# Performance work log

Hardware: AMD Instinct MI355X
Metric: run time of the kernel (lower is better)

## Reference

```python
import jax, jax.numpy as jnp
import numpy as np
from jax import lax

GROUPS = 32
CH = 2048
CG = CH // GROUPS  # 64 channels per group
H = W = 64
B = 4
EPS = 1e-5


def _conv2d(x, w, b, padding, dilation=1):
    # x: [N, Cin, H, W], w: [Cout, Cin, kh, kw] (OIHW)
    y = lax.conv_general_dilated(
        x, w, window_strides=(1, 1),
        padding=[(padding, padding), (padding, padding)],
        rhs_dilation=(dilation, dilation),
        dimension_numbers=("NCHW", "OIHW", "NCHW"))
    return y + b[None, :, None, None]


def _prelu(x, alpha):
    # single shared slope (num_parameters=1)
    return jnp.where(x >= 0, x, alpha[0] * x)


def setup_inputs() -> dict:
    key = jax.random.key(0)
    ks = jax.random.split(key, 6)
    s = 0.05
    f32 = jnp.float32
    return {
        "x": jax.random.normal(ks[0], (B, CH, H, W), f32),
        # EFFM.conv1x1 (on concatenated pooled h/w strips)
        "w_hw": jax.random.normal(ks[1], (CG, CG, 1, 1), f32) * s,
        "b_hw": jnp.zeros((CG,), f32),
        # GroupNorm(cg, cg): per-channel affine
        "gn_w": jnp.ones((CG,), f32),
        "gn_b": jnp.zeros((CG,), f32),
        # RC branch1: 3x3 conv pad=1 + PReLU
        "w_b1": jax.random.normal(ks[2], (CG, CG, 3, 3), f32) * s,
        "b_b1": jnp.zeros((CG,), f32),
        "a_b1": jnp.full((1,), 0.25, f32),
        # RC branch2: 3x3 conv dilation=2 pad=2 + PReLU
        "w_b2": jax.random.normal(ks[3], (CG, CG, 3, 3), f32) * s,
        "b_b2": jnp.zeros((CG,), f32),
        "a_b2": jnp.full((1,), 0.25, f32),
        # RC conv128to64: 1x1 conv 2*cg -> cg
        "w_cat": jax.random.normal(ks[4], (CG, 2 * CG, 1, 1), f32) * s,
        "b_cat": jnp.zeros((CG,), f32),
    }


def _effm(x, w_hw, b_hw, gn_w, gn_b, w_b1, b_b1, a_b1, w_b2, b_b2, a_b2, w_cat, b_cat):
    b, c, h, w = x.shape
    cg = c // GROUPS
    bg = b * GROUPS
    gx = x.reshape(bg, cg, h, w)

    # --- coordinate attention branch ---
    x_h = jnp.mean(gx, axis=3, keepdims=True)                       # [bg, cg, h, 1]
    x_w = jnp.mean(gx, axis=2, keepdims=True).transpose(0, 1, 3, 2)  # [bg, cg, w, 1]
    hw = jnp.concatenate([x_h, x_w], axis=2)                         # [bg, cg, h+w, 1]
    # 1x1 conv == channel mixing linear
    hw = jnp.einsum("oi,bilk->bolk", w_hw[:, :, 0, 0], hw) + b_hw[None, :, None, None]
    x_h, x_w = hw[:, :, :h, :], hw[:, :, h:, :]
    gate = gx * jax.nn.sigmoid(x_h) * jax.nn.sigmoid(x_w.transpose(0, 1, 3, 2))

    # GroupNorm(num_groups=cg, num_channels=cg) == per-channel instance norm
    mu = jnp.mean(gate, axis=(2, 3), keepdims=True)
    var = jnp.var(gate, axis=(2, 3), keepdims=True)
    x1 = (gate - mu) * lax.rsqrt(var + EPS)
    x1 = x1 * gn_w[None, :, None, None] + gn_b[None, :, None, None]

    # --- RC multi-scale branch ---
    br1 = _prelu(_conv2d(gx, w_b1, b_b1, padding=1), a_b1) + gx
    br2 = _prelu(_conv2d(gx, w_b2, b_b2, padding=2, dilation=2), a_b2) + gx
    cat = jnp.concatenate([br1, br2], axis=1)                        # [bg, 2cg, h, w]
    x2 = jnp.einsum("oi,bihw->bohw", w_cat[:, :, 0, 0], cat) + b_cat[None, :, None, None]

    # --- cross softmax-matmul attention ---
    x11 = jax.nn.softmax(jnp.mean(x1, axis=(2, 3)), axis=-1)          # [bg, cg]
    x21 = jax.nn.softmax(jnp.mean(x2, axis=(2, 3)), axis=-1)          # [bg, cg]
    weights = (jnp.einsum("gc,gchw->ghw", x11, x2)
               + jnp.einsum("gc,gchw->ghw", x21, x1))                # [bg, h, w]
    out = gx * jax.nn.sigmoid(weights)[:, None, :, :]
    return out.reshape(b, c, h, w)


def reference(x, w_hw, b_hw, gn_w, gn_b, w_b1, b_b1, a_b1, w_b2, b_b2, a_b2, w_cat, b_cat):
    return _effm(x, w_hw, b_hw, gn_w, gn_b, w_b1, b_b1, a_b1, w_b2, b_b2, a_b2, w_cat, b_cat)
```

## Files before the change

kernel.cpp:

```cpp
#include <hip/hip_runtime.h>
#include <hip/hip_bf16.h>

#define HWPX 4096

typedef __attribute__((ext_vector_type(8))) short short8v;
typedef __attribute__((ext_vector_type(4))) float f32x4;
typedef __attribute__((ext_vector_type(16))) float f32x16;
#define MFMA32(a,b,c) __builtin_amdgcn_mfma_f32_32x32x16_bf16(a,b,c,0,0,0)

__device__ __forceinline__ float sigf(float x){ return 1.0f/(1.0f+__expf(-x)); }
__device__ __forceinline__ unsigned short f2bf(float f){
  __hip_bfloat16 h = __float2bfloat16(f);
  unsigned short u; __builtin_memcpy(&u, &h, sizeof(u)); return u;
}
__device__ __forceinline__ float bf2f(unsigned short u){
  return __uint_as_float(((unsigned)u)<<16);
}
__device__ __forceinline__ void gl2lds16(const void* g, void* l){
  __builtin_amdgcn_global_load_lds((const __attribute__((address_space(1))) void*)g,
                                   (__attribute__((address_space(3))) void*)l, 16, 0, 0);
}

__global__ __launch_bounds__(256) void k_pre(const float* __restrict__ x,
                                             const float* __restrict__ wb1,
                                             const float* __restrict__ wb2,
                                             const float* __restrict__ wcat,
                                             const float* __restrict__ gnb,
                                             unsigned short* __restrict__ xb,
                                             float* __restrict__ hwbuf,
                                             unsigned short* __restrict__ wimg,
                                             unsigned short* __restrict__ wcimg,
                                             float* __restrict__ x11,
                                             float* __restrict__ x2mean){
  int bid = blockIdx.x, tid = threadIdx.x;
  if (bid >= 1088){
    int idx = (bid - 1088)*2048 + tid*8;
    f32x4 z = {0.f,0.f,0.f,0.f};
    *(f32x4*)(x2mean + idx) = z;
    *(f32x4*)(x2mean + idx + 4) = z;
    return;
  }
  if (bid >= 1024){
    int bid2 = bid - 1024;
    for (int idx = bid2*256 + tid; idx < 73728; idx += 64*256){
      int f = idx >> 9, r = idx & 511, lane = r >> 3, j = r & 7;
      int ck = f / 36, rem = f % 36;
      int conv = rem / 18, rem2 = rem % 18;
      int tap = rem2 >> 1, cot = rem2 & 1;
      int co = cot*32 + (lane & 31);
      int ci = ck*16 + (lane >> 5)*8 + j;
      const float* src = conv ? wb2 : wb1;
      wimg[idx] = f2bf(src[(co*64 + ci)*9 + tap]);
    }
    if (bid2 == 0){
      for (int idx = tid; idx < 8192; idx += 256){
        int f = idx >> 9, r = idx & 511, lane = r >> 3, j = r & 7;
        int kfc = f >> 1, cot = f & 1;
        int o = cot*32 + (lane & 31);
        int ch = kfc*16 + (lane >> 5)*8 + j;
        wcimg[idx] = f2bf(wcat[o*128 + ch]);
      }
      if (tid < 64){
        float g = gnb[tid];
        float m = g;
        for (int s=32; s; s>>=1) m = fmaxf(m, __shfl_xor(m, s));
        float e = __expf(g-m);
        float se = e;
        for (int s=32; s; s>>=1) se += __shfl_xor(se, s);
        x11[tid] = e/se;
      }
    }
    return;
  }
  int g = bid >> 3, slot = bid & 7;
  int col = tid & 63, wid = tid >> 6;
  __shared__ float rsm[8*64];
  __shared__ float csm[4*8*64];
  float colacc[8] = {0,0,0,0,0,0,0,0};
  const float* xbase = x + ((size_t)(g*64 + slot*8))*HWPX;
  for (int p=0;p<16;++p){
    int r = wid + 4*p;
    const float* src = xbase + r*64 + col;
    float v[8];
    #pragma unroll
    for (int e=0;e<8;e++) v[e] = src[(size_t)e*HWPX];
    unsigned pk[4];
    #pragma unroll
    for (int j=0;j<4;j++) pk[j] = (unsigned)f2bf(v[2*j]) | ((unsigned)f2bf(v[2*j+1])<<16);
    f32x4 st; __builtin_memcpy(&st, pk, 16);
    *(f32x4*)((char*)xb + (((size_t)(g*64+r))*8 + slot)*1024 + col*16) = st;
    #pragma unroll
    for (int e=0;e<8;e++){
      float s = v[e];
      s += __shfl_xor(s,1); s += __shfl_xor(s,2); s += __shfl_xor(s,4);
      s += __shfl_xor(s,8); s += __shfl_xor(s,16); s += __shfl_xor(s,32);
      if ((tid&63)==0) rsm[e*64+r] = s;
      colacc[e] += v[e];
    }
  }
  #pragma unroll
  for (int e=0;e<8;e++) csm[(wid*8+e)*64+col] = colacc[e];
  __syncthreads();
  float* hb = hwbuf + ((size_t)(g*64 + slot*8))*128;
  for (int idx=tid; idx<512; idx+=256){
    int e = idx>>6, r = idx&63;
    hb[e*128 + r] = rsm[e*64+r] * (1.0f/64.0f);
  }
  for (int idx=tid; idx<512; idx+=256){
    int e = idx>>6, c2 = idx&63;
    float s = csm[(0*8+e)*64+c2] + csm[(1*8+e)*64+c2] + csm[(2*8+e)*64+c2] + csm[(3*8+e)*64+c2];
    hb[e*128 + 64 + c2] = s * (1.0f/64.0f);
  }
}

__global__ __launch_bounds__(256) void k_hwmm(const float* hwbuf, const float* whw,
                                              const float* bhw, float* sigbuf){
  int g = blockIdx.x;
  __shared__ float hl[64*128];
  int tid = threadIdx.x;
  const float* src = hwbuf + (size_t)g*8192;
  for (int i = tid; i < 2048; i += 256) ((float4*)hl)[i] = ((const float4*)src)[i];
  __syncthreads();
  int p  = tid & 127;
  int o0 = (tid >> 7) * 32;
  float acc[32];
  #pragma unroll
  for (int k=0;k<32;k++) acc[k] = bhw[o0+k];
  for (int i=0;i<64;i++){
    float v = hl[i*128+p];
    #pragma unroll
    for (int k=0;k<32;k++) acc[k] = fmaf(whw[(o0+k)*64+i], v, acc[k]);
  }
  float* dst = sigbuf + (size_t)g*8192;
  #pragma unroll
  for (int k=0;k<32;k++) dst[(o0+k)*128+p] = sigf(acc[k]);
}

__global__ __launch_bounds__(256) void k_gate2(const unsigned short* __restrict__ xb,
                                               const float* __restrict__ sigbuf,
                                               const float* __restrict__ gnw,
                                               const float* __restrict__ gnb,
                                               float* __restrict__ scsh){
  int bsw = (blockIdx.x & 7)*(gridDim.x >> 3) + (blockIdx.x >> 3);
  int g = bsw >> 3, slot = bsw & 7;
  int tid = threadIdx.x, col = tid & 63, wq = tid >> 6, lane = tid & 63;
  __shared__ float srm[8*64], scm[8*64], red[4*16];
  for (int idx = tid; idx < 1024; idx += 256){
    int e = idx >> 7, k = idx & 127;
    float v = sigbuf[(size_t)g*8192 + (size_t)(slot*8+e)*128 + k];
    if (k < 64) srm[e*64+k] = v; else scm[e*64+k-64] = v;
  }
  __syncthreads();
  float s[8] = {0,0,0,0,0,0,0,0}, s2[8] = {0,0,0,0,0,0,0,0};
  const char* base = (const char*)xb + (((size_t)(g*64))*8 + slot)*1024;
  for (int p=0;p<16;++p){
    int row = wq*16 + p;
    short8v xv = *(const short8v*)(base + (size_t)row*8192 + col*16);
    #pragma unroll
    for (int e=0;e<8;e++){
      float v = bf2f((unsigned short)xv[e]) * srm[e*64+row] * scm[e*64+col];
      s[e] += v; s2[e] = fmaf(v, v, s2[e]);
    }
  }
  #pragma unroll
  for (int e=0;e<8;e++){
    #pragma unroll
    for (int off=1; off<64; off<<=1){ s[e] += __shfl_xor(s[e], off); s2[e] += __shfl_xor(s2[e], off); }
  }
  if (lane == 0){
    #pragma unroll
    for (int e=0;e<8;e++){ red[wq*16+e] = s[e]; red[wq*16+8+e] = s2[e]; }
  }
  __syncthreads();
  if (tid < 8){
    float S  = red[tid]   + red[16+tid] + red[32+tid] + red[48+tid];
    float S2 = red[8+tid] + red[24+tid] + red[40+tid] + red[56+tid];
    float mu = S*(1.f/4096.f);
    float var = S2*(1.f/4096.f) - mu*mu;
    int c = slot*8 + tid;
    float scale = rsqrtf(var + 1e-5f) * gnw[c];
    scsh[(g*64+c)*2]   = scale;
    scsh[(g*64+c)*2+1] = gnb[c] - mu*scale;
  }
}

template<int DIL>
__device__ __forceinline__ void conv_compute(const char* INq, const char* WLq,
                                             int ch2, int rquad, int l31, int lh, int lane,
                                             f32x16 acc[2][4]){
  constexpr int NROW = 4 + 2*DIL;
  constexpr int conv = DIL - 1;
  #pragma unroll
  for (int dxx=0; dxx<3; ++dxx){
    const int colb = ch2*32 + l31 + (dxx-1)*DIL + 2;
    short8v Brow[NROW];
    #pragma unroll
    for (int i=0; i<NROW; ++i){
      int rowi = rquad*4 + i + 2 - DIL;
      Brow[i] = *(const short8v*)(INq + (rowi*2 + lh)*1088 + colb*16);
    }
    #pragma unroll
    for (int dyy=0; dyy<3; ++dyy){
      int tap = dyy*3 + dxx;
      const char* wp = WLq + (size_t)((conv*9 + tap)*2)*1024 + lane*16;
      short8v A0 = *(const short8v*)(wp);
      short8v A1 = *(const short8v*)(wp + 1024);
      #pragma unroll
      for (int pt=0; pt<4; ++pt){
        acc[0][pt] = MFMA32(A0, Brow[pt + dyy*DIL], acc[0][pt]);
        acc[1][pt] = MFMA32(A1, Brow[pt + dyy*DIL], acc[1][pt]);
      }
    }
  }
}

__global__ __launch_bounds__(512) void k_convcat(const unsigned short* __restrict__ xb,
                                                 const char* __restrict__ wgl,
                                                 const char* __restrict__ wcgl,
                                                 const float* __restrict__ bb1,
                                                 const float* __restrict__ bb2,
                                                 const float* __restrict__ a1p,
                                                 const float* __restrict__ a2p,
                                                 const float* __restrict__ bcat,
                                                 const float* __restrict__ x11,
                                                 float* __restrict__ wsum2,
                                                 float* __restrict__ x2mean){
  extern __shared__ char smem[];
  char* BRL = smem;
  char* WCL = smem + 131072;
  float* x11l = (float*)(smem + 147456);
  float* bcl  = x11l + 64;

  const int tid = threadIdx.x;
  const int bsw = (blockIdx.x & 7)*(gridDim.x >> 3) + (blockIdx.x >> 3);
  const int g = bsw >> 3;
  const int strip = bsw & 7;
  const int r0 = strip*8;
  const int w = tid >> 6;
  const int lane = tid & 63;
  const int l31 = lane & 31;
  const int lh  = lane >> 5;
  const int conv = w >> 2;
  const int ch2 = (w >> 1) & 1;
  const int rquad = w & 1;

  if (tid < 64){ x11l[tid] = x11[tid]; bcl[tid] = bcat[tid]; }
  if (tid < 192){
    int b = tid / 96, t = tid % 96;
    int seg = t >> 2, pc = t & 3;
    int colp = (pc < 2) ? pc : pc + 64;
    *(f32x4*)(smem + b*26112 + seg*1088 + colp*16) = (f32x4){0.f,0.f,0.f,0.f};
  }
  #pragma unroll
  for (int k=0;k<2;k++){
    int idx = tid + k*512;
    gl2lds16(wcgl + (size_t)idx*16, WCL + idx*16);
  }

  f32x16 acc[2][4];
  #pragma unroll
  for (int cot=0;cot<2;cot++)
    #pragma unroll
    for (int pt=0;pt<4;pt++)
      #pragma unroll
      for (int e=0;e<16;e++) acc[cot][pt][e] = 0.f;

  auto stage_chunk = [&](int ck, char* inb, char* wb){
    #pragma unroll
    for (int k=0;k<4;k++){
      int idx = tid + k*512;
      gl2lds16(wgl + (size_t)ck*36864 + (size_t)idx*16, wb + idx*16);
    }
    if (tid < 256){
      int idx = 2048 + tid;
      gl2lds16(wgl + (size_t)ck*36864 + (size_t)idx*16, wb + idx*16);
    }
    #pragma unroll
    for (int i=0;i<3;++i){
      int seg = w*3 + i;
      int row = seg >> 1, slot = seg & 1;
      int rg = r0 - 2 + row;
      char* dst = inb + seg*1088 + 32 + lane*16;
      if ((unsigned)rg < 64u){
        gl2lds16((const char*)xb + (((size_t)(g*64+rg))*8 + ck*2 + slot)*1024 + lane*16, dst);
      } else {
        *(f32x4*)dst = (f32x4){0.f,0.f,0.f,0.f};
      }
    }
  };

  stage_chunk(0, smem, smem + 52224);
  __syncthreads();

  #pragma unroll
  for (int ck=0; ck<4; ++ck){
    if (ck < 3)
      stage_chunk(ck+1, smem + ((ck+1)&1)*26112, smem + 52224 + ((ck+1)&1)*36864);
    const char* inq = smem + (ck&1)*26112;
    const char* wq  = smem + 52224 + (ck&1)*36864;
    if (conv == 0) conv_compute<1>(inq, wq, ch2, rquad, l31, lh, lane, acc);
    else           conv_compute<2>(inq, wq, ch2, rquad, l31, lh, lane, acc);
    __syncthreads();
  }

  {
    const float alpha = conv ? a2p[0] : a1p[0];
    const float* bbp = conv ? bb2 : bb1;
    #pragma unroll
    for (int cot=0;cot<2;++cot){
      #pragma unroll
      for (int rq=0;rq<4;++rq){
        int co0 = cot*32 + 8*rq + 4*lh;
        float b0 = bbp[co0], b1 = bbp[co0+1], b2 = bbp[co0+2], b3 = bbp[co0+3];
        int ch0 = conv*64 + co0;
        #pragma unroll
        for (int pt=0;pt<4;++pt){
          int prow = rquad*4 + pt;
          int colg = ch2*32 + l31;
          const char* rsrc = (const char*)xb + (((size_t)(g*64 + r0 + prow))*8 + (co0>>3))*1024
                             + colg*16 + (co0&7)*2;
          ushort4 rv = *(const ushort4*)rsrc;
          float v0 = acc[cot][pt][rq*4+0] + b0; v0 = (v0>=0.f? v0 : alpha*v0) + bf2f(rv.x);
          float v1 = acc[cot][pt][rq*4+1] + b1; v1 = (v1>=0.f? v1 : alpha*v1) + bf2f(rv.y);
          float v2 = acc[cot][pt][rq*4+2] + b2; v2 = (v2>=0.f? v2 : alpha*v2) + bf2f(rv.z);
          float v3 = acc[cot][pt][rq*4+3] + b3; v3 = (v3>=0.f? v3 : alpha*v3) + bf2f(rv.w);
          int px = prow*64 + colg;
          int addr = (px*256 + ch0*2) ^ ((px & 15) << 4);
          ushort4 pk; pk.x=f2bf(v0); pk.y=f2bf(v1); pk.z=f2bf(v2); pk.w=f2bf(v3);
          *(ushort4*)(BRL + addr) = pk;
        }
      }
    }
  }
  __syncthreads();

  {
    f32x16 c2[2][2];
    #pragma unroll
    for (int cot=0;cot<2;cot++)
      #pragma unroll
      for (int t=0;t<2;t++)
        #pragma unroll
        for (int e=0;e<16;e++) c2[cot][t][e] = 0.f;

    #pragma unroll
    for (int kfc=0;kfc<8;++kfc){
      const char* ap = WCL + (size_t)(kfc*2)*1024 + lane*16;
      short8v A0 = *(const short8v*)(ap);
      short8v A1 = *(const short8v*)(ap + 1024);
      #pragma unroll
      for (int t=0;t<2;++t){
        int px = w*64 + t*32 + l31;
        int addr = (px*256 + kfc*32 + lh*16) ^ ((px & 15) << 4);
        short8v B = *(const short8v*)(BRL + addr);
        c2[0][t] = MFMA32(A0, B, c2[0][t]);
        c2[1][t] = MFMA32(A1, B, c2[1][t]);
      }
    }
    float u0 = 0.f, u1 = 0.f;
    #pragma unroll
    for (int cot=0;cot<2;++cot){
      #pragma unroll
      for (int reg=0;reg<16;++reg){
        int o = cot*32 + (reg&3) + 8*(reg>>2) + 4*lh;
        float xw = x11l[o], bc = bcl[o];
        u0 += xw*(c2[cot][0][reg] + bc);
        u1 += xw*(c2[cot][1][reg] + bc);
        float sv = c2[cot][0][reg] + c2[cot][1][reg];
        sv += __shfl_xor(sv, 1); sv += __shfl_xor(sv, 2);
        sv += __shfl_xor(sv, 4); sv += __shfl_xor(sv, 8); sv += __shfl_xor(sv, 16);
        if (l31 == 0) atomicAdd(&x2mean[g*64 + o], sv);
      }
    }
    u0 += __shfl_xor(u0, 32);
    u1 += __shfl_xor(u1, 32);
    if (lh == 0){
      float* wp2 = wsum2 + (size_t)g*4096 + strip*512 + w*64 + l31;
      wp2[0]  = u0;
      wp2[32] = u1;
    }
  }
}

__global__ __launch_bounds__(256) void k_final2(const float* __restrict__ x,
                                                const float* __restrict__ sigbuf,
                                                const float* __restrict__ scsh,
                                                const float* __restrict__ x2mean,
                                                const float* __restrict__ bcat,
                                                const float* __restrict__ wsum2,
                                                float* __restrict__ out){
  int blk = blockIdx.x;
  int g = blk >> 4, chunk = blk & 15;
  int tid = threadIdx.x;
  __shared__ float x21s[64];
  __shared__ float crow[64*4];
  __shared__ float ccol[64*64];
  __shared__ float Ssm;
  const float* sgb = sigbuf + (size_t)g*8192;
  if (tid < 64){
    float mean = x2mean[g*64 + tid] * (1.f/4096.f) + bcat[tid];
    float mx = mean;
    for (int s=32; s; s>>=1) mx = fmaxf(mx, __shfl_xor(mx, s));
    float e = __expf(mean - mx);
    float se = e;
    for (int s=32; s; s>>=1) se += __shfl_xor(se, s);
    x21s[tid] = e/se;
  }
  for (int idx = tid; idx < 4096; idx += 256){
    int c = idx >> 6, col = idx & 63;
    ccol[idx] = sgb[c*128 + 64 + col];
  }
  __syncthreads();
  {
    int c = tid >> 2, rr = tid & 3;
    crow[tid] = x21s[c] * scsh[(g*64+c)*2] * sgb[c*128 + chunk*4 + rr];
  }
  if (tid < 64){
    float v = x21s[tid] * scsh[(g*64+tid)*2+1];
    for (int s=32; s; s>>=1) v += __shfl_xor(v, s);
    if (tid == 0) Ssm = v;
  }
  __syncthreads();
  int px = chunk*256 + tid;
  int rr = tid >> 6, col = tid & 63;
  const float* xp = x + (size_t)(g*64)*HWPX + px;
  float W = wsum2[(size_t)g*4096 + px] + Ssm;
  float xv[64];
  #pragma unroll
  for (int c=0;c<64;c++){
    xv[c] = xp[(size_t)c*HWPX];
    W = fmaf(crow[c*4+rr]*ccol[c*64+col], xv[c], W);
  }
  float s = sigf(W);
  float* op = out + (size_t)(g*64)*HWPX + px;
  #pragma unroll
  for (int c=0;c<64;c++){
    op[(size_t)c*HWPX] = xv[c] * s;
  }
}

extern "C" void kernel_launch(void* const* d_in, const int* in_sizes, int n_in,
                              void* d_out, int out_size, void* d_ws, size_t ws_size,
                              hipStream_t stream) {
  const float* x     = (const float*)d_in[0];
  const float* w_hw  = (const float*)d_in[1];
  const float* b_hw  = (const float*)d_in[2];
  const float* gn_w  = (const float*)d_in[3];
  const float* gn_b  = (const float*)d_in[4];
  const float* w_b1  = (const float*)d_in[5];
  const float* b_b1  = (const float*)d_in[6];
  const float* a_b1  = (const float*)d_in[7];
  const float* w_b2  = (const float*)d_in[8];
  const float* b_b2  = (const float*)d_in[9];
  const float* a_b2  = (const float*)d_in[10];
  const float* w_cat = (const float*)d_in[11];
  const float* b_cat = (const float*)d_in[12];

  char* ws = (char*)d_ws;
  unsigned short* wimg  = (unsigned short*)(ws + 0);
  unsigned short* wcimg = (unsigned short*)(ws + 147456);
  float* x11    = (float*)(ws + 163840);
  float* x2mean = (float*)(ws + 164096);
  float* scsh   = (float*)(ws + 196864);
  float* wsum2  = (float*)(ws + 262400);
  float* hwbuf  = (float*)(ws + 2359552);
  float* sigb   = (float*)(ws + 6553856);
  unsigned short* xb = (unsigned short*)d_out;
  float* out = (float*)d_out;

  hipFuncSetAttribute(reinterpret_cast<const void*>(k_convcat),
                      hipFuncAttributeMaxDynamicSharedMemorySize, 147968);

  k_pre  <<<1092, 256, 0, stream>>>(x, w_b1, w_b2, w_cat, gn_b, xb, hwbuf, wimg, wcimg,
                                    x11, x2mean);
  k_hwmm <<<128,  256, 0, stream>>>(hwbuf, w_hw, b_hw, sigb);
  k_gate2<<<1024, 256, 0, stream>>>(xb, sigb, gn_w, gn_b, scsh);
  k_convcat<<<1024, 512, 147968, stream>>>(xb, (const char*)wimg, (const char*)wcimg,
                                           b_b1, b_b2, a_b1, a_b2, b_cat, x11, wsum2, x2mean);
  k_final2<<<2048, 256, 0, stream>>>(x, sigb, scsh, x2mean, b_cat, wsum2, out);
}
```

Baseline: 287.4 us.

## Load conv weights from global into registers instead of staging through LDS

Result: no change. 288.8 us (+0.5%).

```diff
diff --git a/kernel.cpp b/kernel.cpp
--- a/kernel.cpp
+++ b/kernel.cpp
@@ -19,6 +19,11 @@
 __device__ __forceinline__ void gl2lds16(const void* g, void* l){
   __builtin_amdgcn_global_load_lds((const __attribute__((address_space(1))) void*)g,
                                    (__attribute__((address_space(3))) void*)l, 16, 0, 0);
+}
+template<int CTRL>
+__device__ __forceinline__ float dpp_add(float v){
+  int t = __builtin_amdgcn_update_dpp(0, __float_as_int(v), CTRL, 0xf, 0xf, true);
+  return v + __int_as_float(t);
 }
 
 __global__ __launch_bounds__(256) void k_pre(const float* __restrict__ x,
@@ -185,31 +190,18 @@
 }
 
 template<int DIL>
-__device__ __forceinline__ void conv_compute(const char* INq, const char* WLq,
-                                             int ch2, int rquad, int l31, int lh, int lane,
-                                             f32x16 acc[2][4]){
+__device__ __forceinline__ void conv_group(const char* ib, const short8v (&Ag)[3][2],
+                                           f32x16 (&acc)[2][4]){
   constexpr int NROW = 4 + 2*DIL;
-  constexpr int conv = DIL - 1;
-  #pragma unroll
-  for (int dxx=0; dxx<3; ++dxx){
-    const int colb = ch2*32 + l31 + (dxx-1)*DIL + 2;
-    short8v Brow[NROW];
-    #pragma unroll
-    for (int i=0; i<NROW; ++i){
-      int rowi = rquad*4 + i + 2 - DIL;
-      Brow[i] = *(const short8v*)(INq + (rowi*2 + lh)*1088 + colb*16);
-    }
-    #pragma unroll
-    for (int dyy=0; dyy<3; ++dyy){
-      int tap = dyy*3 + dxx;
-      const char* wp = WLq + (size_t)((conv*9 + tap)*2)*1024 + lane*16;
-      short8v A0 = *(const short8v*)(wp);
-      short8v A1 = *(const short8v*)(wp + 1024);
-      #pragma unroll
-      for (int pt=0; pt<4; ++pt){
-        acc[0][pt] = MFMA32(A0, Brow[pt + dyy*DIL], acc[0][pt]);
-        acc[1][pt] = MFMA32(A1, Brow[pt + dyy*DIL], acc[1][pt]);
-      }
+  short8v Brow[NROW];
+  #pragma unroll
+  for (int i=0;i<NROW;++i) Brow[i] = *(const short8v*)(ib + i*2176);
+  #pragma unroll
+  for (int dyy=0;dyy<3;++dyy){
+    #pragma unroll
+    for (int pt=0;pt<4;++pt){
+      acc[0][pt] = MFMA32(Ag[dyy][0], Brow[pt + dyy*DIL], acc[0][pt]);
+      acc[1][pt] = MFMA32(Ag[dyy][1], Brow[pt + dyy*DIL], acc[1][pt]);
     }
   }
 }
@@ -227,8 +219,7 @@
                                                  float* __restrict__ x2mean){
   extern __shared__ char smem[];
   char* BRL = smem;
-  char* WCL = smem + 131072;
-  float* x11l = (float*)(smem + 147456);
+  float* x11l = (float*)(smem + 131072);
   float* bcl  = x11l + 64;
 
   const int tid = threadIdx.x;
@@ -243,6 +234,7 @@
   const int conv = w >> 2;
   const int ch2 = (w >> 1) & 1;
   const int rquad = w & 1;
+  const int dil = conv + 1;
 
   if (tid < 64){ x11l[tid] = x11[tid]; bcl[tid] = bcat[tid]; }
   if (tid < 192){
@@ -251,56 +243,69 @@
     int colp = (pc < 2) ? pc : pc + 64;
     *(f32x4*)(smem + b*26112 + seg*1088 + colp*16) = (f32x4){0.f,0.f,0.f,0.f};
   }
-  #pragma unroll
-  for (int k=0;k<2;k++){
-    int idx = tid + k*512;
-    gl2lds16(wcgl + (size_t)idx*16, WCL + idx*16);
-  }
-
-  f32x16 acc[2][4];
-  #pragma unroll
-  for (int cot=0;cot<2;cot++)
-    #pragma unroll
-    for (int pt=0;pt<4;pt++)
-      #pragma unroll
-      for (int e=0;e<16;e++) acc[cot][pt][e] = 0.f;
-
-  auto stage_chunk = [&](int ck, char* inb, char* wb){
-    #pragma unroll
-    for (int k=0;k<4;k++){
-      int idx = tid + k*512;
-      gl2lds16(wgl + (size_t)ck*36864 + (size_t)idx*16, wb + idx*16);
-    }
-    if (tid < 256){
-      int idx = 2048 + tid;
-      gl2lds16(wgl + (size_t)ck*36864 + (size_t)idx*16, wb + idx*16);
-    }
+
+  auto stage = [&](int ck, char* inb){
     #pragma unroll
     for (int i=0;i<3;++i){
       int seg = w*3 + i;
       int row = seg >> 1, slot = seg & 1;
       int rg = r0 - 2 + row;
       char* dst = inb + seg*1088 + 32 + lane*16;
-      if ((unsigned)rg < 64u){
+      if ((unsigned)rg < 64u)
         gl2lds16((const char*)xb + (((size_t)(g*64+rg))*8 + ck*2 + slot)*1024 + lane*16, dst);
-      } else {
+      else
         *(f32x4*)dst = (f32x4){0.f,0.f,0.f,0.f};
-      }
     }
   };
 
-  stage_chunk(0, smem, smem + 52224);
-  __syncthreads();
-
-  #pragma unroll
-  for (int ck=0; ck<4; ++ck){
-    if (ck < 3)
-      stage_chunk(ck+1, smem + ((ck+1)&1)*26112, smem + 52224 + ((ck+1)&1)*36864);
+  f32x16 acc[2][4];
+  #pragma unroll
+  for (int cot=0;cot<2;cot++)
+    #pragma unroll
+    for (int pt=0;pt<4;pt++)
+      #pragma unroll
+      for (int e=0;e<16;e++) acc[cot][pt][e] = 0.f;
+
+  const char* wconv = wgl + conv*18432 + lane*16;
+  short8v Abuf[2][3][2];
+  #pragma unroll
+  for (int dyy=0;dyy<3;++dyy)
+    #pragma unroll
+    for (int cot=0;cot<2;++cot)
+      Abuf[0][dyy][cot] = *(const short8v*)(wconv + (dyy*3+0)*2048 + cot*1024);
+
+  stage(0, smem);
+  __syncthreads();
+  stage(1, smem + 26112);
+
+  #pragma unroll
+  for (int gi=0; gi<12; ++gi){
+    const int ck = gi/3, dxx = gi%3;
+    if (gi < 11){
+      const int ck2 = (gi+1)/3, dx2 = (gi+1)%3;
+      #pragma unroll
+      for (int dyy=0;dyy<3;++dyy)
+        #pragma unroll
+        for (int cot=0;cot<2;++cot)
+          Abuf[(gi+1)&1][dyy][cot] =
+            *(const short8v*)(wconv + ck2*36864 + (dyy*3+dx2)*2048 + cot*1024);
+    }
     const char* inq = smem + (ck&1)*26112;
-    const char* wq  = smem + 52224 + (ck&1)*36864;
-    if (conv == 0) conv_compute<1>(inq, wq, ch2, rquad, l31, lh, lane, acc);
-    else           conv_compute<2>(inq, wq, ch2, rquad, l31, lh, lane, acc);
-    __syncthreads();
+    const char* ib = inq + ((rquad*4 + 2 - dil)*2 + lh)*1088
+                     + (ch2*32 + l31 + 2 + (dxx-1)*dil)*16;
+    if (conv == 0) conv_group<1>(ib, Abuf[gi&1], acc);
+    else           conv_group<2>(ib, Abuf[gi&1], acc);
+    if (dxx == 2){
+      __syncthreads();
+      if (ck < 2) stage(ck+2, smem + (ck&1)*26112);
+    }
+  }
+
+  short8v Ac0[8], Ac1[8];
+  #pragma unroll
+  for (int kfc=0;kfc<8;++kfc){
+    Ac0[kfc] = *(const short8v*)(wcgl + (size_t)(kfc*2+0)*1024 + lane*16);
+    Ac1[kfc] = *(const short8v*)(wcgl + (size_t)(kfc*2+1)*1024 + lane*16);
   }
 
   {
@@ -345,16 +350,13 @@
 
     #pragma unroll
     for (int kfc=0;kfc<8;++kfc){
-      const char* ap = WCL + (size_t)(kfc*2)*1024 + lane*16;
-      short8v A0 = *(const short8v*)(ap);
-      short8v A1 = *(const short8v*)(ap + 1024);
       #pragma unroll
       for (int t=0;t<2;++t){
         int px = w*64 + t*32 + l31;
         int addr = (px*256 + kfc*32 + lh*16) ^ ((px & 15) << 4);
         short8v B = *(const short8v*)(BRL + addr);
-        c2[0][t] = MFMA32(A0, B, c2[0][t]);
-        c2[1][t] = MFMA32(A1, B, c2[1][t]);
+        c2[0][t] = MFMA32(Ac0[kfc], B, c2[0][t]);
+        c2[1][t] = MFMA32(Ac1[kfc], B, c2[1][t]);
       }
     }
     float u0 = 0.f, u1 = 0.f;
@@ -367,9 +369,12 @@
         u0 += xw*(c2[cot][0][reg] + bc);
         u1 += xw*(c2[cot][1][reg] + bc);
         float sv = c2[cot][0][reg] + c2[cot][1][reg];
-        sv += __shfl_xor(sv, 1); sv += __shfl_xor(sv, 2);
-        sv += __shfl_xor(sv, 4); sv += __shfl_xor(sv, 8); sv += __shfl_xor(sv, 16);
-        if (l31 == 0) atomicAdd(&x2mean[g*64 + o], sv);
+        sv = dpp_add<0x111>(sv);
+        sv = dpp_add<0x112>(sv);
+        sv = dpp_add<0x114>(sv);
+        sv = dpp_add<0x118>(sv);
+        sv = dpp_add<0x142>(sv);
+        if ((lane & 31) == 31) atomicAdd(&x2mean[g*64 + o], sv);
       }
     }
     u0 += __shfl_xor(u0, 32);
@@ -469,13 +474,13 @@
   float* out = (float*)d_out;
 
   hipFuncSetAttribute(reinterpret_cast<const void*>(k_convcat),
-                      hipFuncAttributeMaxDynamicSharedMemorySize, 147968);
+                      hipFuncAttributeMaxDynamicSharedMemorySize, 131584);
 
   k_pre  <<<1092, 256, 0, stream>>>(x, w_b1, w_b2, w_cat, gn_b, xb, hwbuf, wimg, wcimg,
                                     x11, x2mean);
   k_hwmm <<<128,  256, 0, stream>>>(hwbuf, w_hw, b_hw, sigb);
   k_gate2<<<1024, 256, 0, stream>>>(xb, sigb, gn_w, gn_b, scsh);
-  k_convcat<<<1024, 512, 147968, stream>>>(xb, (const char*)wimg, (const char*)wcimg,
+  k_convcat<<<1024, 512, 131584, stream>>>(xb, (const char*)wimg, (const char*)wcimg,
                                            b_b1, b_b2, a_b1, a_b2, b_cat, x11, wsum2, x2mean);
   k_final2<<<2048, 256, 0, stream>>>(x, sigb, scsh, x2mean, b_cat, wsum2, out);
 }
```

## Stage conv inputs in two 32-channel halves instead of double-buffered 16-channel chunks

Applied to the files above, without the earlier changes.

After: 293.8 us. +2.2%, slower.

```diff
diff --git a/kernel.cpp b/kernel.cpp
--- a/kernel.cpp
+++ b/kernel.cpp
@@ -44,11 +44,10 @@
     int bid2 = bid - 1024;
     for (int idx = bid2*256 + tid; idx < 73728; idx += 64*256){
       int f = idx >> 9, r = idx & 511, lane = r >> 3, j = r & 7;
-      int ck = f / 36, rem = f % 36;
-      int conv = rem / 18, rem2 = rem % 18;
-      int tap = rem2 >> 1, cot = rem2 & 1;
+      int qc = f / 36, rem = f % 36, tap = rem >> 2, kc = rem & 3;
+      int q = qc >> 1, conv = qc & 1, kf = kc >> 1, cot = kc & 1;
       int co = cot*32 + (lane & 31);
-      int ci = ck*16 + (lane >> 5)*8 + j;
+      int ci = q*32 + kf*16 + (lane >> 5)*8 + j;
       const float* src = conv ? wb2 : wb1;
       wimg[idx] = f2bf(src[(co*64 + ci)*9 + tap]);
     }
@@ -184,36 +183,6 @@
   }
 }
 
-template<int DIL>
-__device__ __forceinline__ void conv_compute(const char* INq, const char* WLq,
-                                             int ch2, int rquad, int l31, int lh, int lane,
-                                             f32x16 acc[2][4]){
-  constexpr int NROW = 4 + 2*DIL;
-  constexpr int conv = DIL - 1;
-  #pragma unroll
-  for (int dxx=0; dxx<3; ++dxx){
-    const int colb = ch2*32 + l31 + (dxx-1)*DIL + 2;
-    short8v Brow[NROW];
-    #pragma unroll
-    for (int i=0; i<NROW; ++i){
-      int rowi = rquad*4 + i + 2 - DIL;
-      Brow[i] = *(const short8v*)(INq + (rowi*2 + lh)*1088 + colb*16);
-    }
-    #pragma unroll
-    for (int dyy=0; dyy<3; ++dyy){
-      int tap = dyy*3 + dxx;
-      const char* wp = WLq + (size_t)((conv*9 + tap)*2)*1024 + lane*16;
-      short8v A0 = *(const short8v*)(wp);
-      short8v A1 = *(const short8v*)(wp + 1024);
-      #pragma unroll
-      for (int pt=0; pt<4; ++pt){
-        acc[0][pt] = MFMA32(A0, Brow[pt + dyy*DIL], acc[0][pt]);
-        acc[1][pt] = MFMA32(A1, Brow[pt + dyy*DIL], acc[1][pt]);
-      }
-    }
-  }
-}
-
 __global__ __launch_bounds__(512) void k_convcat(const unsigned short* __restrict__ xb,
                                                  const char* __restrict__ wgl,
                                                  const char* __restrict__ wcgl,
@@ -226,6 +195,8 @@
                                                  float* __restrict__ wsum2,
                                                  float* __restrict__ x2mean){
   extern __shared__ char smem[];
+  char* INL = smem;
+  char* WL  = smem + 52224;
   char* BRL = smem;
   char* WCL = smem + 131072;
   float* x11l = (float*)(smem + 147456);
@@ -243,19 +214,19 @@
   const int conv = w >> 2;
   const int ch2 = (w >> 1) & 1;
   const int rquad = w & 1;
-
-  if (tid < 64){ x11l[tid] = x11[tid]; bcl[tid] = bcat[tid]; }
-  if (tid < 192){
-    int b = tid / 96, t = tid % 96;
-    int seg = t >> 2, pc = t & 3;
-    int colp = (pc < 2) ? pc : pc + 64;
-    *(f32x4*)(smem + b*26112 + seg*1088 + colp*16) = (f32x4){0.f,0.f,0.f,0.f};
-  }
+  const int dil = conv + 1;
+
   #pragma unroll
   for (int k=0;k<2;k++){
     int idx = tid + k*512;
     gl2lds16(wcgl + (size_t)idx*16, WCL + idx*16);
   }
+  if (tid < 64){ x11l[tid] = x11[tid]; bcl[tid] = bcat[tid]; }
+  if (tid < 192){
+    int seg = tid >> 2, pc = tid & 3;
+    int colp = (pc < 2) ? pc : pc + 64;
+    *(f32x4*)(INL + seg*1088 + colp*16) = (f32x4){0.f,0.f,0.f,0.f};
+  }
 
   f32x16 acc[2][4];
   #pragma unroll
@@ -265,43 +236,47 @@
       #pragma unroll
       for (int e=0;e<16;e++) acc[cot][pt][e] = 0.f;
 
-  auto stage_chunk = [&](int ck, char* inb, char* wb){
-    #pragma unroll
-    for (int k=0;k<4;k++){
+  for (int q=0;q<2;++q){
+    if (q) __syncthreads();
+    #pragma unroll
+    for (int k=0;k<9;k++){
       int idx = tid + k*512;
-      gl2lds16(wgl + (size_t)ck*36864 + (size_t)idx*16, wb + idx*16);
-    }
-    if (tid < 256){
-      int idx = 2048 + tid;
-      gl2lds16(wgl + (size_t)ck*36864 + (size_t)idx*16, wb + idx*16);
-    }
-    #pragma unroll
-    for (int i=0;i<3;++i){
-      int seg = w*3 + i;
-      int row = seg >> 1, slot = seg & 1;
+      gl2lds16(wgl + (size_t)q*73728 + (size_t)idx*16, WL + idx*16);
+    }
+    #pragma unroll
+    for (int i=0;i<6;++i){
+      int seg = w*6 + i;
+      int row = seg >> 2, slot = seg & 3;
       int rg = r0 - 2 + row;
-      char* dst = inb + seg*1088 + 32 + lane*16;
+      char* dst = INL + seg*1088 + 32;
       if ((unsigned)rg < 64u){
-        gl2lds16((const char*)xb + (((size_t)(g*64+rg))*8 + ck*2 + slot)*1024 + lane*16, dst);
+        const char* src = (const char*)xb + ((((size_t)(g*64+rg))*8) + q*4 + slot)*1024 + lane*16;
+        gl2lds16(src, dst + lane*16);
       } else {
-        *(f32x4*)dst = (f32x4){0.f,0.f,0.f,0.f};
-      }
-    }
-  };
-
-  stage_chunk(0, smem, smem + 52224);
-  __syncthreads();
-
-  #pragma unroll
-  for (int ck=0; ck<4; ++ck){
-    if (ck < 3)
-      stage_chunk(ck+1, smem + ((ck+1)&1)*26112, smem + 52224 + ((ck+1)&1)*36864);
-    const char* inq = smem + (ck&1)*26112;
-    const char* wq  = smem + 52224 + (ck&1)*36864;
-    if (conv == 0) conv_compute<1>(inq, wq, ch2, rquad, l31, lh, lane, acc);
-    else           conv_compute<2>(inq, wq, ch2, rquad, l31, lh, lane, acc);
+        *(f32x4*)(dst + lane*16) = (f32x4){0.f,0.f,0.f,0.f};
+      }
+    }
     __syncthreads();
-  }
+    #pragma unroll
+    for (int tap=0;tap<9;++tap){
+      const int dy = tap/3 - 1, dx = tap%3 - 1;
+      #pragma unroll
+      for (int kf=0;kf<2;++kf){
+        const char* wp = WL + (size_t)(((conv*9+tap)*4 + kf*2)*1024) + lane*16;
+        short8v A0 = *(const short8v*)(wp);
+        short8v A1 = *(const short8v*)(wp + 1024);
+        const char* ib = INL + (kf*2 + lh)*1088 + (ch2*32 + 2 + l31 + dx*dil)*16;
+        #pragma unroll
+        for (int pt=0;pt<4;++pt){
+          int rowin = rquad*4 + pt + dy*dil + 2;
+          short8v B = *(const short8v*)(ib + rowin*4352);
+          acc[0][pt] = MFMA32(A0, B, acc[0][pt]);
+          acc[1][pt] = MFMA32(A1, B, acc[1][pt]);
+        }
+      }
+    }
+  }
+  __syncthreads();
 
   {
     const float alpha = conv ? a2p[0] : a1p[0];
```
